# Performance work log

Measured on AMD Instinct MI355X. Metric: run time of the kernel, lower is better.

## Reference

```python
import jax, jax.numpy as jnp
import numpy as np
from jax import lax

TEMP = 65.0
CLIP_DIST = 0.01
EPS = 1e-6  # torch PairwiseDistance eps (added to the difference) and log eps
NTOKEN, NINP, NHID = 32000, 1024, 1024
SEQ_LEN, BSZ, NSAMPLES = 128, 64, 10


def setup_inputs() -> dict:
    key = jax.random.key(0)
    ks = jax.random.split(key, 7)
    data = jax.random.randint(ks[0], (SEQ_LEN, BSZ), 0, NTOKEN)
    samples = jax.random.randint(ks[1], (NSAMPLES, SEQ_LEN * BSZ), 0, NTOKEN)
    # encoder init_weights: uniform(-0.1, 0.1); RNN weights small to avoid tanh saturation
    emb_W = jax.random.uniform(ks[2], (NTOKEN, NINP), minval=-0.1, maxval=0.1, dtype=jnp.float32)
    W_ih = jax.random.normal(ks[3], (NHID, NINP), dtype=jnp.float32) * 0.03
    b_ih = jax.random.normal(ks[4], (NHID,), dtype=jnp.float32) * 0.01
    W_hh = jax.random.normal(ks[5], (NHID, NHID), dtype=jnp.float32) * 0.03
    b_hh = jax.random.normal(ks[6], (NHID,), dtype=jnp.float32) * 0.01
    return {"data": data, "samples": samples, "emb_W": emb_W,
            "W_ih": W_ih, "b_ih": b_ih, "W_hh": W_hh, "b_hh": b_hh}


def _sq_pdist(x, y):
    # torch PairwiseDistance(p=2).pow(2): ||x - y + eps||^2 (no sqrt needed)
    d = x - y + EPS
    return jnp.sum(d * d, axis=-1)


def reference(data, samples, emb_W, W_ih, b_ih, W_hh, b_hh):
    seq_len, bsz = data.shape
    nhid = W_hh.shape[0]
    emb = emb_W[data]                                  # [S, B, ninp]
    h0 = jnp.zeros((bsz, nhid), dtype=emb_W.dtype)

    def step(h, e):
        h_new = jnp.tanh(e @ W_ih.T + b_ih + h @ W_hh.T + b_hh)
        return h_new, h_new

    _, outs = lax.scan(step, h0, emb)                  # [S, B, H]
    raw = jnp.concatenate([h0[None], outs], axis=0)    # [S+1, B, H]

    # positive term: temp * ||h_t - h_{t+1}||^2, summed, averaged over seq_len
    pos = TEMP * _sq_pdist(raw[:-1], raw[1:])          # [S, B]
    loss = pos.sum() / seq_len

    prev = raw[:-1].reshape(seq_len * bsz, nhid)       # [S*B, H]
    samples_emb = emb_W[samples]                       # [ns, S*B, ninp]
    samples_W = samples_emb @ W_ih.T + b_ih            # [ns, S*B, H]
    hiddens_U = prev @ W_hh.T + b_hh                   # [S*B, H]

    out = jnp.tanh(samples_W + hiddens_U[None])        # [ns, S*B, H]
    dist = _sq_pdist(prev[None], out)                  # [ns, S*B]
    dist = jnp.clip(dist, 0.0, CLIP_DIST)
    n = seq_len * bsz
    sum_of_exp = jnp.sum(jnp.exp(-dist), axis=0) / n   # [S*B]
    loss = loss + jnp.log(sum_of_exp + EPS).sum()
    return loss
```

## Files before the change

### kernel.cpp

```cpp
#include <hip/hip_runtime.h>
#include <hip/hip_bf16.h>
#include <cmath>

typedef __bf16 bf16;
typedef __attribute__((ext_vector_type(8))) __bf16 bf16x8;
typedef __attribute__((ext_vector_type(4))) __bf16 bf16x4;
typedef __attribute__((ext_vector_type(4))) float f32x4;
typedef unsigned long long ull;

#define TEMPC 65.0f
#define EPSC 1e-6f

#define GLD_LDS16(gptr, lptr)                                                             \
    __builtin_amdgcn_global_load_lds(                                                     \
        (const __attribute__((address_space(1))) unsigned int*)(gptr),                    \
        (__attribute__((address_space(3))) unsigned int*)(lptr), 16, 0, 0)

__global__ void conv3_kernel(const float* __restrict__ e, bf16* __restrict__ eb,
                             const float* __restrict__ a, bf16* __restrict__ ab,
                             const float* __restrict__ b, bf16* __restrict__ bb)
{
    const int base   = (blockIdx.x * blockDim.x + threadIdx.x) * 4;
    const int stride = gridDim.x * blockDim.x * 4;
    for (int i = base; i < 32000 * 1024; i += stride) {
        const float4 v = *(const float4*)(e + i);
        bf16x4 o; o[0]=(bf16)v.x; o[1]=(bf16)v.y; o[2]=(bf16)v.z; o[3]=(bf16)v.w;
        *(bf16x4*)(eb + i) = o;
    }
    for (int i = base; i < 1024 * 1024; i += stride) {
        const float4 v = *(const float4*)(a + i);
        bf16x4 o; o[0]=(bf16)v.x; o[1]=(bf16)v.y; o[2]=(bf16)v.z; o[3]=(bf16)v.w;
        *(bf16x4*)(ab + i) = o;
    }
    for (int i = base; i < 1024 * 1024; i += stride) {
        const float4 v = *(const float4*)(b + i);
        bf16x4 o; o[0]=(bf16)v.x; o[1]=(bf16)v.y; o[2]=(bf16)v.z; o[3]=(bf16)v.w;
        *(bf16x4*)(bb + i) = o;
    }
}

__global__ __launch_bounds__(256, 1)
void fused_kernel(const int* __restrict__ data, const bf16* __restrict__ emb,
                  const bf16* __restrict__ Wih, const float* __restrict__ bih,
                  bf16* __restrict__ P, bf16* __restrict__ raw,
                  const bf16* __restrict__ Whh, bf16* __restrict__ XWb,
                  const float* __restrict__ bhh, bf16* __restrict__ Ust,
                  int* __restrict__ cnt, float* __restrict__ lacc)
{
    __shared__ __align__(16) char pool[147584];
    const int tid = threadIdx.x;
    const int l   = tid & 63;
    const int w   = tid >> 6;
    const int id  = blockIdx.x;

    if (id < 128) {
        bf16* Wlds = (bf16*)pool;
        char* Hlds = pool + 131072;
        const int group  = id & 7;
        const int slot   = id >> 3;
        const int jbase  = slot * 64;
        const int frow   = l & 15;
        const int kchunk = l >> 4;
        const int jglob  = jbase + w * 16 + frow;
        const int rr     = frow & 7;

        {
            const int jloc = l >> 2;
            const int csw  = ((l & 3) ^ ((l >> 3) & 3)) * 16;
            const char* gsrc = (const char*)Whh + (size_t)(jbase + w * 16 + jloc) * 2048 + csw;
            for (int kk = 0; kk < 32; ++kk)
                GLD_LDS16(gsrc + kk * 64, Wlds + (kk * 4 + w) * 512);
            asm volatile("s_waitcnt vmcnt(0)" ::: "memory");
            __syncthreads();
        }
        const float bh = bhh[jglob];

        const int ksw   = kchunk ^ ((frow >> 1) & 3);
        const bf16* wrd = Wlds + w * 512 + frow * 32 + ksw * 8;
        const char* hrd = Hlds + rr * 2064 + kchunk * 16;
        const int jpair = jglob & ~1;
        float posacc = 0.f;

        for (int t = 0; t < 128; ++t) {
            if (t > 0) {
                if (tid < 4)
                    while (__hip_atomic_load(&cnt[((t * 8 + group) * 4 + tid) * 32],
                                             __ATOMIC_RELAXED, __HIP_MEMORY_SCOPE_AGENT) < 4)
                        __builtin_amdgcn_s_sleep(1);
                __syncthreads();
            }
            const ull* hsrc8 = (const ull*)(raw + (size_t)t * 65536 + group * 8192);
            ull hv[8];
            #pragma unroll
            for (int i = 0; i < 8; ++i)
                hv[i] = __hip_atomic_load(hsrc8 + tid + i * 256,
                                          __ATOMIC_RELAXED, __HIP_MEMORY_SCOPE_AGENT);
            unsigned int xww[4];
            #pragma unroll
            for (int r = 0; r < 4; ++r) {
                const int bc = (kchunk * 4 + r) & 7;
                const size_t row = (size_t)(t * 64 + group * 8 + bc);
                xww[r] = __hip_atomic_load((const unsigned int*)(XWb + row * 1024 + jpair),
                                           __ATOMIC_RELAXED, __HIP_MEMORY_SCOPE_AGENT);
            }
            #pragma unroll
            for (int i = 0; i < 8; ++i)
                *(ull*)(Hlds + i * 2064 + tid * 8) = hv[i];
            __syncthreads();

            f32x4 acc0 = {0.f,0.f,0.f,0.f}, acc1 = {0.f,0.f,0.f,0.f};
            #pragma unroll
            for (int kk = 0; kk < 32; kk += 2) {
                bf16x8 a0 = *(const bf16x8*)(hrd + kk * 64);
                bf16x8 a1 = *(const bf16x8*)(hrd + kk * 64 + 64);
                acc0 = __builtin_amdgcn_mfma_f32_16x16x32_bf16(a0, *(const bf16x8*)(wrd + kk * 2048),       acc0, 0, 0, 0);
                acc1 = __builtin_amdgcn_mfma_f32_16x16x32_bf16(a1, *(const bf16x8*)(wrd + (kk + 1) * 2048), acc1, 0, 0, 0);
            }

            for (;;) {
                bool bad = false;
                #pragma unroll
                for (int r = 0; r < 4; ++r) bad |= (xww[r] == 0xFFFFFFFFu);
                if (!bad) break;
                #pragma unroll
                for (int r = 0; r < 4; ++r)
                    if (xww[r] == 0xFFFFFFFFu) {
                        const int bc = (kchunk * 4 + r) & 7;
                        const size_t row = (size_t)(t * 64 + group * 8 + bc);
                        xww[r] = __hip_atomic_load((const unsigned int*)(XWb + row * 1024 + jpair),
                                                   __ATOMIC_RELAXED, __HIP_MEMORY_SCOPE_AGENT);
                    }
            }

            bf16* rawN = raw + (size_t)(t + 1) * 65536;
            if (l < 32) {
                #pragma unroll
                for (int r = 0; r < 4; ++r) {
                    const int b = (l >> 4) * 4 + r;
                    const unsigned short x16 = (jglob & 1) ? (unsigned short)(xww[r] >> 16)
                                                           : (unsigned short)(xww[r] & 0xFFFF);
                    const float xwv = __builtin_bit_cast(float, (unsigned int)x16 << 16);
                    const float V = acc0[r] + acc1[r] + bh;
                    const float h = tanhf(xwv + V);
                    const size_t row = (size_t)(t * 64 + group * 8 + b);
                    Ust[row * 1024 + jglob] = (bf16)V;
                    const bf16 hb = (bf16)h;
                    const float ht = (float)*(const bf16*)(Hlds + b * 2064 + jglob * 2);
                    const float pd = ht - (float)hb + EPSC;
                    posacc += pd * pd;
                    unsigned short hs = __builtin_bit_cast(unsigned short, hb);
                    unsigned short hn = (unsigned short)__shfl_down((int)hs, 1, 64);
                    if ((frow & 1) == 0) {
                        unsigned int pack = (unsigned int)hs | ((unsigned int)hn << 16);
                        unsigned int* dst = (unsigned int*)(rawN + (size_t)(group * 8 + b) * 1024 + jglob);
                        __hip_atomic_store(dst, pack, __ATOMIC_RELAXED, __HIP_MEMORY_SCOPE_AGENT);
                    }
                }
            }
            if (t < 127) {
                __syncthreads();
                if (tid == 0)
                    __hip_atomic_fetch_add(&cnt[(((t + 1) * 8 + group) * 4 + (slot & 3)) * 32], 1,
                                           __ATOMIC_RELAXED, __HIP_MEMORY_SCOPE_AGENT);
            }
        }
        #pragma unroll
        for (int off2 = 32; off2 > 0; off2 >>= 1) posacc += __shfl_down(posacc, off2, 64);
        if (l == 0) atomicAdd(lacc, posacc * (TEMPC / 128.f));
    } else {
        bf16* As = (bf16*)pool;
        bf16* Bs = (bf16*)(pool + 16384);
        const int wr = w >> 1, wc = w & 1;
        const bool isXW = (id < 640);

        int mbase, nbase;
        const char *Asrc0, *Asrc1;
        const int r0 = w * 32 + (l >> 2);
        const int csw = ((l & 3) ^ ((l >> 3) & 3)) * 16;
        if (isXW) {
            const int q = id - 128;
            mbase = (q >> 3) * 128;
            nbase = (q & 7) * 128;
            Asrc0 = (const char*)emb + (size_t)data[mbase + r0] * 2048 + csw;
            Asrc1 = (const char*)emb + (size_t)data[mbase + r0 + 16] * 2048 + csw;
        } else {
            const int q  = id - 640;
            const int wg = (q & 7) * 250 + (q >> 3);
            mbase = (wg >> 3) * 128;
            nbase = (wg & 7) * 128;
            Asrc0 = (const char*)emb + (size_t)(mbase + r0) * 2048 + csw;
            Asrc1 = (const char*)emb + (size_t)(mbase + r0 + 16) * 2048 + csw;
        }
        const char* Bsrc0 = (const char*)Wih + (size_t)(nbase + r0) * 2048 + csw;
        const char* Bsrc1 = (const char*)Wih + (size_t)(nbase + r0 + 16) * 2048 + csw;

        const int frow  = l & 15;
        const int koffE = (((l >> 4) ^ ((frow >> 1) & 3)) * 8);
        const bf16* Ard = As + (wr * 64 + frow) * 32 + koffE;
        const bf16* Brd = Bs + (wc * 64 + frow) * 32 + koffE;

        auto stage = [&](int buf, int kb) {
            bf16* As_ = As + buf * 4096 + w * 1024;
            bf16* Bs_ = Bs + buf * 4096 + w * 1024;
            GLD_LDS16(Asrc0 + kb, As_);
            GLD_LDS16(Asrc1 + kb, As_ + 512);
            GLD_LDS16(Bsrc0 + kb, Bs_);
            GLD_LDS16(Bsrc1 + kb, Bs_ + 512);
        };

        stage(0, 0);
        stage(1, 64);

        f32x4 acc[4][4] = {};
        for (int k = 0; k < 32; ++k) {
            if (k == 31) asm volatile("s_waitcnt vmcnt(0)" ::: "memory");
            else         asm volatile("s_waitcnt vmcnt(4)" ::: "memory");
            __builtin_amdgcn_s_barrier();
            const bf16* Ab = Ard + (k & 1) * 4096;
            const bf16* Bb = Brd + (k & 1) * 4096;
            bf16x8 af[4], bfr[4];
            #pragma unroll
            for (int mt = 0; mt < 4; ++mt) af[mt]  = *(const bf16x8*)(Ab + mt * 16 * 32);
            #pragma unroll
            for (int nt = 0; nt < 4; ++nt) bfr[nt] = *(const bf16x8*)(Bb + nt * 16 * 32);
            #pragma unroll
            for (int mt = 0; mt < 4; ++mt)
                #pragma unroll
                for (int nt = 0; nt < 4; ++nt)
                    acc[mt][nt] = __builtin_amdgcn_mfma_f32_16x16x32_bf16(af[mt], bfr[nt], acc[mt][nt], 0, 0, 0);
            asm volatile("s_waitcnt lgkmcnt(0)" ::: "memory");
            __builtin_amdgcn_s_barrier();
            if (k + 2 < 32) stage(k & 1, (k + 2) * 64);
        }

        if (isXW) {
            #pragma unroll
            for (int mt = 0; mt < 4; ++mt)
                #pragma unroll
                for (int nt = 0; nt < 4; ++nt) {
                    const int colg = nbase + wc * 64 + nt * 16 + frow;
                    const float bi = bih[colg];
                    #pragma unroll
                    for (int r = 0; r < 4; ++r) {
                        const int rowg = mbase + wr * 64 + mt * 16 + (l >> 4) * 4 + r;
                        const bf16 vb = (bf16)(acc[mt][nt][r] + bi);
                        unsigned short vs = __builtin_bit_cast(unsigned short, vb);
                        unsigned short vn = (unsigned short)__shfl_down((int)vs, 1, 64);
                        if ((frow & 1) == 0) {
                            unsigned int pack = (unsigned int)vs | ((unsigned int)vn << 16);
                            __hip_atomic_store((unsigned int*)(XWb + (size_t)rowg * 1024 + colg),
                                               pack, __ATOMIC_RELAXED, __HIP_MEMORY_SCOPE_AGENT);
                        }
                    }
                }
        } else {
            #pragma unroll
            for (int mt = 0; mt < 4; ++mt)
                #pragma unroll
                for (int nt = 0; nt < 4; ++nt) {
                    const int colg = nbase + wc * 64 + nt * 16 + frow;
                    const float bi = bih[colg];
                    #pragma unroll
                    for (int r = 0; r < 4; ++r) {
                        const int rowg = mbase + wr * 64 + mt * 16 + (l >> 4) * 4 + r;
                        P[(size_t)rowg * 1024 + colg] = (bf16)(acc[mt][nt][r] + bi);
                    }
                }
        }
    }
}

__global__ __launch_bounds__(256)
void neg_kernel(const int* __restrict__ samples, const bf16* __restrict__ P,
                const bf16* __restrict__ Ust, const bf16* __restrict__ raw,
                float* __restrict__ lacc)
{
    const int l = threadIdx.x & 63;
    const int r = blockIdx.x * 4 + (threadIdx.x >> 6);
    const bf16* u  = Ust + (size_t)r * 1024;
    const bf16* pv = raw + (size_t)r * 1024;

    float uf[16], vf[16];
    {
        bf16x8 u0 = *(const bf16x8*)(u + l * 8);
        bf16x8 u1 = *(const bf16x8*)(u + 512 + l * 8);
        bf16x8 v0 = *(const bf16x8*)(pv + l * 8);
        bf16x8 v1 = *(const bf16x8*)(pv + 512 + l * 8);
        #pragma unroll
        for (int i = 0; i < 8; ++i) {
            uf[i] = (float)u0[i]; uf[8 + i] = (float)u1[i];
            vf[i] = (float)v0[i]; vf[8 + i] = (float)v1[i];
        }
    }

    float se = 0.f;
    #pragma unroll
    for (int s = 0; s < 10; ++s) {
        const int tok = samples[s * 8192 + r];
        const bf16* pr = P + (size_t)tok * 1024;
        bf16x8 p0 = *(const bf16x8*)(pr + l * 8);
        bf16x8 p1 = *(const bf16x8*)(pr + 512 + l * 8);
        float d2 = 0.f;
        #pragma unroll
        for (int i = 0; i < 8; ++i) {
            const float o0 = tanhf((float)p0[i] + uf[i]);
            const float d0 = vf[i] - o0 + EPSC;
            d2 += d0 * d0;
            const float o1 = tanhf((float)p1[i] + uf[8 + i]);
            const float d1 = vf[8 + i] - o1 + EPSC;
            d2 += d1 * d1;
        }
        #pragma unroll
        for (int off = 1; off < 64; off <<= 1)
            d2 += __shfl_xor(d2, off, 64);
        se += expf(-fminf(d2, 0.01f));
    }
    if (l == 0) atomicAdd(lacc, logf(se * (1.f / 8192.f) + EPSC));
}

__global__ void fin_kernel(const float* __restrict__ lacc, float* __restrict__ out)
{
    if (threadIdx.x == 0) out[0] = lacc[0];
}

extern "C" void kernel_launch(void* const* d_in, const int* in_sizes, int n_in,
                              void* d_out, int out_size, void* d_ws, size_t ws_size,
                              hipStream_t stream)
{
    const int*   data    = (const int*)d_in[0];
    const int*   samples = (const int*)d_in[1];
    const float* emb     = (const float*)d_in[2];
    const float* Wih     = (const float*)d_in[3];
    const float* bih     = (const float*)d_in[4];
    const float* Whh     = (const float*)d_in[5];
    const float* bhh     = (const float*)d_in[6];

    char* ws = (char*)d_ws;
    size_t off = 0;
    auto alloc = [&](size_t bytes) { void* p = ws + off; off += (bytes + 255) & ~(size_t)255; return p; };
    bf16*  emb_b = (bf16*)alloc((size_t)32000 * 1024 * 2);
    bf16*  Wih_b = (bf16*)alloc((size_t)1024 * 1024 * 2);
    bf16*  Whh_b = (bf16*)alloc((size_t)1024 * 1024 * 2);
    bf16*  P     = (bf16*)alloc((size_t)32000 * 1024 * 2);
    bf16*  XWb   = (bf16*)alloc((size_t)8192 * 1024 * 2);
    bf16*  Ust   = (bf16*)alloc((size_t)8192 * 1024 * 2);
    bf16*  raw   = (bf16*)alloc((size_t)129 * 64 * 1024 * 2);
    float* lacc  = (float*)alloc(256);
    int*   cnt   = (int*)alloc(524288);

    hipMemsetAsync(raw, 0, 64 * 1024 * 2, stream);
    hipMemsetAsync(XWb, 0xFF, (size_t)8192 * 1024 * 2, stream);
    hipMemsetAsync(lacc, 0, 256, stream);
    hipMemsetAsync(cnt,  0, 524288, stream);

    conv3_kernel<<<2048, 256, 0, stream>>>(emb, emb_b, Wih, Wih_b, Whh, Whh_b);

    fused_kernel<<<2640, 256, 0, stream>>>(data, emb_b, Wih_b, bih, P,
                                           raw, Whh_b, XWb, bhh, Ust, cnt, lacc);

    neg_kernel<<<2048, 256, 0, stream>>>(samples, P, Ust, raw, lacc);

    fin_kernel<<<1, 64, 0, stream>>>(lacc, (float*)d_out);
}
```

Before: 577.2 us.

## Fuse embedding bf16 conversion into GEMM loads and negative-sampling into persistent kernel

After: 615.3 us. 1.07x slower.

```diff
diff --git a/kernel.cpp b/kernel.cpp
--- a/kernel.cpp
+++ b/kernel.cpp
@@ -10,42 +10,44 @@
 
 #define TEMPC 65.0f
 #define EPSC 1e-6f
+#define PD_OFF 200000
 
 #define GLD_LDS16(gptr, lptr)                                                             \
     __builtin_amdgcn_global_load_lds(                                                     \
         (const __attribute__((address_space(1))) unsigned int*)(gptr),                    \
         (__attribute__((address_space(3))) unsigned int*)(lptr), 16, 0, 0)
 
-__global__ void conv3_kernel(const float* __restrict__ e, bf16* __restrict__ eb,
-                             const float* __restrict__ a, bf16* __restrict__ ab,
+__device__ __forceinline__ bf16x8 ald16(const bf16* p)
+{
+    union { ull u[2]; bf16x8 v; } c;
+    c.u[0] = __hip_atomic_load((const ull*)p,     __ATOMIC_RELAXED, __HIP_MEMORY_SCOPE_AGENT);
+    c.u[1] = __hip_atomic_load((const ull*)p + 1, __ATOMIC_RELAXED, __HIP_MEMORY_SCOPE_AGENT);
+    return c.v;
+}
+
+__global__ void conv2_kernel(const float* __restrict__ a, bf16* __restrict__ ab,
                              const float* __restrict__ b, bf16* __restrict__ bb)
 {
-    const int base   = (blockIdx.x * blockDim.x + threadIdx.x) * 4;
+    int i = (blockIdx.x * blockDim.x + threadIdx.x) * 4;
     const int stride = gridDim.x * blockDim.x * 4;
-    for (int i = base; i < 32000 * 1024; i += stride) {
-        const float4 v = *(const float4*)(e + i);
-        bf16x4 o; o[0]=(bf16)v.x; o[1]=(bf16)v.y; o[2]=(bf16)v.z; o[3]=(bf16)v.w;
-        *(bf16x4*)(eb + i) = o;
+    for (; i < 1024 * 1024; i += stride) {
+        const float4 va = *(const float4*)(a + i);
+        bf16x4 oa; oa[0]=(bf16)va.x; oa[1]=(bf16)va.y; oa[2]=(bf16)va.z; oa[3]=(bf16)va.w;
+        *(bf16x4*)(ab + i) = oa;
+        const float4 vb = *(const float4*)(b + i);
+        bf16x4 ob; ob[0]=(bf16)vb.x; ob[1]=(bf16)vb.y; ob[2]=(bf16)vb.z; ob[3]=(bf16)vb.w;
+        *(bf16x4*)(bb + i) = ob;
     }
-    for (int i = base; i < 1024 * 1024; i += stride) {
-        const float4 v = *(const float4*)(a + i);
-        bf16x4 o; o[0]=(bf16)v.x; o[1]=(bf16)v.y; o[2]=(bf16)v.z; o[3]=(bf16)v.w;
-        *(bf16x4*)(ab + i) = o;
-    }
-    for (int i = base; i < 1024 * 1024; i += stride) {
-        const float4 v = *(const float4*)(b + i);
-        bf16x4 o; o[0]=(bf16)v.x; o[1]=(bf16)v.y; o[2]=(bf16)v.z; o[3]=(bf16)v.w;
-        *(bf16x4*)(bb + i) = o;
-    }
 }
 
 __global__ __launch_bounds__(256, 1)
-void fused_kernel(const int* __restrict__ data, const bf16* __restrict__ emb,
-                  const bf16* __restrict__ Wih, const float* __restrict__ bih,
-                  bf16* __restrict__ P, bf16* __restrict__ raw,
-                  const bf16* __restrict__ Whh, bf16* __restrict__ XWb,
-                  const float* __restrict__ bhh, bf16* __restrict__ Ust,
-                  int* __restrict__ cnt, float* __restrict__ lacc)
+void fused_kernel(const int* __restrict__ data, const int* __restrict__ samples,
+                  const float* __restrict__ embf, const bf16* __restrict__ Wih,
+                  const float* __restrict__ bih, bf16* __restrict__ P,
+                  bf16* __restrict__ raw, const bf16* __restrict__ Whh,
+                  bf16* __restrict__ XWb, const float* __restrict__ bhh,
+                  bf16* __restrict__ Ust, int* __restrict__ cnt,
+                  float* __restrict__ lacc)
 {
     __shared__ __align__(16) char pool[147584];
     const int tid = threadIdx.x;
@@ -143,79 +145,97 @@
                     const float V = acc0[r] + acc1[r] + bh;
                     const float h = tanhf(xwv + V);
                     const size_t row = (size_t)(t * 64 + group * 8 + b);
-                    Ust[row * 1024 + jglob] = (bf16)V;
+                    const bf16 ub = (bf16)V;
                     const bf16 hb = (bf16)h;
                     const float ht = (float)*(const bf16*)(Hlds + b * 2064 + jglob * 2);
                     const float pd = ht - (float)hb + EPSC;
                     posacc += pd * pd;
+                    unsigned short us = __builtin_bit_cast(unsigned short, ub);
                     unsigned short hs = __builtin_bit_cast(unsigned short, hb);
+                    unsigned short un = (unsigned short)__shfl_down((int)us, 1, 64);
                     unsigned short hn = (unsigned short)__shfl_down((int)hs, 1, 64);
                     if ((frow & 1) == 0) {
-                        unsigned int pack = (unsigned int)hs | ((unsigned int)hn << 16);
-                        unsigned int* dst = (unsigned int*)(rawN + (size_t)(group * 8 + b) * 1024 + jglob);
-                        __hip_atomic_store(dst, pack, __ATOMIC_RELAXED, __HIP_MEMORY_SCOPE_AGENT);
+                        unsigned int up = (unsigned int)us | ((unsigned int)un << 16);
+                        unsigned int hp = (unsigned int)hs | ((unsigned int)hn << 16);
+                        __hip_atomic_store((unsigned int*)(Ust + row * 1024 + jglob), up,
+                                           __ATOMIC_RELAXED, __HIP_MEMORY_SCOPE_AGENT);
+                        __hip_atomic_store((unsigned int*)(rawN + (size_t)(group * 8 + b) * 1024 + jglob), hp,
+                                           __ATOMIC_RELAXED, __HIP_MEMORY_SCOPE_AGENT);
                     }
                 }
             }
-            if (t < 127) {
-                __syncthreads();
-                if (tid == 0)
-                    __hip_atomic_fetch_add(&cnt[(((t + 1) * 8 + group) * 4 + (slot & 3)) * 32], 1,
-                                           __ATOMIC_RELAXED, __HIP_MEMORY_SCOPE_AGENT);
-            }
+            __syncthreads();
+            if (tid == 0)
+                __hip_atomic_fetch_add(&cnt[(((t + 1) * 8 + group) * 4 + (slot & 3)) * 32], 1,
+                                       __ATOMIC_RELAXED, __HIP_MEMORY_SCOPE_AGENT);
         }
         #pragma unroll
         for (int off2 = 32; off2 > 0; off2 >>= 1) posacc += __shfl_down(posacc, off2, 64);
         if (l == 0) atomicAdd(lacc, posacc * (TEMPC / 128.f));
-    } else {
+    } else if (id < 2640) {
         bf16* As = (bf16*)pool;
         bf16* Bs = (bf16*)(pool + 16384);
         const int wr = w >> 1, wc = w & 1;
         const bool isXW = (id < 640);
 
         int mbase, nbase;
-        const char *Asrc0, *Asrc1;
-        const int r0 = w * 32 + (l >> 2);
-        const int csw = ((l & 3) ^ ((l >> 3) & 3)) * 16;
+        const int rla = w * 32 + (l >> 2);
+        const int g8  = ((l & 3) ^ ((l >> 3) & 3)) * 8;
+        const float *Af0, *Af1;
         if (isXW) {
             const int q = id - 128;
             mbase = (q >> 3) * 128;
             nbase = (q & 7) * 128;
-            Asrc0 = (const char*)emb + (size_t)data[mbase + r0] * 2048 + csw;
-            Asrc1 = (const char*)emb + (size_t)data[mbase + r0 + 16] * 2048 + csw;
+            Af0 = embf + (size_t)data[mbase + rla] * 1024 + g8;
+            Af1 = embf + (size_t)data[mbase + rla + 16] * 1024 + g8;
         } else {
             const int q  = id - 640;
             const int wg = (q & 7) * 250 + (q >> 3);
             mbase = (wg >> 3) * 128;
             nbase = (wg & 7) * 128;
-            Asrc0 = (const char*)emb + (size_t)(mbase + r0) * 2048 + csw;
-            Asrc1 = (const char*)emb + (size_t)(mbase + r0 + 16) * 2048 + csw;
-        }
-        const char* Bsrc0 = (const char*)Wih + (size_t)(nbase + r0) * 2048 + csw;
-        const char* Bsrc1 = (const char*)Wih + (size_t)(nbase + r0 + 16) * 2048 + csw;
-
-        const int frow  = l & 15;
-        const int koffE = (((l >> 4) ^ ((frow >> 1) & 3)) * 8);
-        const bf16* Ard = As + (wr * 64 + frow) * 32 + koffE;
-        const bf16* Brd = Bs + (wc * 64 + frow) * 32 + koffE;
-
-        auto stage = [&](int buf, int kb) {
-            bf16* As_ = As + buf * 4096 + w * 1024;
+            Af0 = embf + (size_t)(mbase + rla) * 1024 + g8;
+            Af1 = embf + (size_t)(mbase + rla + 16) * 1024 + g8;
+        }
+        const int csw = ((l & 3) ^ ((l >> 3) & 3)) * 16;
+        const char* Bsrc0 = (const char*)Wih + (size_t)(nbase + rla) * 2048 + csw;
+        const char* Bsrc1 = (const char*)Wih + (size_t)(nbase + rla + 16) * 2048 + csw;
+        char* Adst = (char*)As + w * 2048 + l * 16;
+
+        float4 fa00, fa01, fa10, fa11;
+        auto issueA = [&](int k) {
+            const float* s0 = Af0 + k * 32;
+            const float* s1 = Af1 + k * 32;
+            fa00 = *(const float4*)s0;  fa01 = *(const float4*)(s0 + 4);
+            fa10 = *(const float4*)s1;  fa11 = *(const float4*)(s1 + 4);
+        };
+        auto writeA = [&](int buf) {
+            bf16x8 o0, o1;
+            o0[0]=(bf16)fa00.x; o0[1]=(bf16)fa00.y; o0[2]=(bf16)fa00.z; o0[3]=(bf16)fa00.w;
+            o0[4]=(bf16)fa01.x; o0[5]=(bf16)fa01.y; o0[6]=(bf16)fa01.z; o0[7]=(bf16)fa01.w;
+            o1[0]=(bf16)fa10.x; o1[1]=(bf16)fa10.y; o1[2]=(bf16)fa10.z; o1[3]=(bf16)fa10.w;
+            o1[4]=(bf16)fa11.x; o1[5]=(bf16)fa11.y; o1[6]=(bf16)fa11.z; o1[7]=(bf16)fa11.w;
+            *(bf16x8*)(Adst + buf * 8192) = o0;
+            *(bf16x8*)(Adst + buf * 8192 + 1024) = o1;
+        };
+        auto stageB = [&](int buf, int kb) {
             bf16* Bs_ = Bs + buf * 4096 + w * 1024;
-            GLD_LDS16(Asrc0 + kb, As_);
-            GLD_LDS16(Asrc1 + kb, As_ + 512);
             GLD_LDS16(Bsrc0 + kb, Bs_);
             GLD_LDS16(Bsrc1 + kb, Bs_ + 512);
         };
 
-        stage(0, 0);
-        stage(1, 64);
+        const int frow  = l & 15;
+        const int koffE = ((l >> 4) ^ ((frow >> 1) & 3)) * 8;
+        const bf16* Ard = As + (wr * 64 + frow) * 32 + koffE;
+        const bf16* Brd = Bs + (wc * 64 + frow) * 32 + koffE;
+
+        issueA(0);
+        stageB(0, 0);
+        writeA(0);
+        __syncthreads();
 
         f32x4 acc[4][4] = {};
         for (int k = 0; k < 32; ++k) {
-            if (k == 31) asm volatile("s_waitcnt vmcnt(0)" ::: "memory");
-            else         asm volatile("s_waitcnt vmcnt(4)" ::: "memory");
-            __builtin_amdgcn_s_barrier();
+            if (k + 1 < 32) { issueA(k + 1); stageB((k + 1) & 1, (k + 1) * 64); }
             const bf16* Ab = Ard + (k & 1) * 4096;
             const bf16* Bb = Brd + (k & 1) * 4096;
             bf16x8 af[4], bfr[4];
@@ -228,94 +248,95 @@
                 #pragma unroll
                 for (int nt = 0; nt < 4; ++nt)
                     acc[mt][nt] = __builtin_amdgcn_mfma_f32_16x16x32_bf16(af[mt], bfr[nt], acc[mt][nt], 0, 0, 0);
-            asm volatile("s_waitcnt lgkmcnt(0)" ::: "memory");
-            __builtin_amdgcn_s_barrier();
-            if (k + 2 < 32) stage(k & 1, (k + 2) * 64);
-        }
-
-        if (isXW) {
-            #pragma unroll
-            for (int mt = 0; mt < 4; ++mt)
-                #pragma unroll
-                for (int nt = 0; nt < 4; ++nt) {
-                    const int colg = nbase + wc * 64 + nt * 16 + frow;
-                    const float bi = bih[colg];
-                    #pragma unroll
-                    for (int r = 0; r < 4; ++r) {
-                        const int rowg = mbase + wr * 64 + mt * 16 + (l >> 4) * 4 + r;
-                        const bf16 vb = (bf16)(acc[mt][nt][r] + bi);
-                        unsigned short vs = __builtin_bit_cast(unsigned short, vb);
-                        unsigned short vn = (unsigned short)__shfl_down((int)vs, 1, 64);
-                        if ((frow & 1) == 0) {
-                            unsigned int pack = (unsigned int)vs | ((unsigned int)vn << 16);
-                            __hip_atomic_store((unsigned int*)(XWb + (size_t)rowg * 1024 + colg),
-                                               pack, __ATOMIC_RELAXED, __HIP_MEMORY_SCOPE_AGENT);
-                        }
+            if (k + 1 < 32) writeA((k + 1) & 1);
+            __syncthreads();
+        }
+
+        #pragma unroll
+        for (int mt = 0; mt < 4; ++mt)
+            #pragma unroll
+            for (int nt = 0; nt < 4; ++nt) {
+                const int colg = nbase + wc * 64 + nt * 16 + frow;
+                const float bi = bih[colg];
+                #pragma unroll
+                for (int r = 0; r < 4; ++r) {
+                    const int rowg = mbase + wr * 64 + mt * 16 + (l >> 4) * 4 + r;
+                    const bf16 vb = (bf16)(acc[mt][nt][r] + bi);
+                    unsigned short vs = __builtin_bit_cast(unsigned short, vb);
+                    unsigned short vn = (unsigned short)__shfl_down((int)vs, 1, 64);
+                    if ((frow & 1) == 0) {
+                        unsigned int pack = (unsigned int)vs | ((unsigned int)vn << 16);
+                        bf16* dstbuf = isXW ? XWb : P;
+                        __hip_atomic_store((unsigned int*)(dstbuf + (size_t)rowg * 1024 + colg),
+                                           pack, __ATOMIC_RELAXED, __HIP_MEMORY_SCOPE_AGENT);
                     }
                 }
-        } else {
-            #pragma unroll
-            for (int mt = 0; mt < 4; ++mt)
-                #pragma unroll
-                for (int nt = 0; nt < 4; ++nt) {
-                    const int colg = nbase + wc * 64 + nt * 16 + frow;
-                    const float bi = bih[colg];
-                    #pragma unroll
-                    for (int r = 0; r < 4; ++r) {
-                        const int rowg = mbase + wr * 64 + mt * 16 + (l >> 4) * 4 + r;
-                        P[(size_t)rowg * 1024 + colg] = (bf16)(acc[mt][nt][r] + bi);
-                    }
+            }
+        if (!isXW) {
+            __syncthreads();
+            if (tid == 0)
+                __hip_atomic_fetch_add(&cnt[PD_OFF], 1,
+                                       __ATOMIC_RELAXED, __HIP_MEMORY_SCOPE_AGENT);
+        }
+    } else {
+        const int n  = id - 2640;
+        const int r0 = n * 16;
+        const int t  = r0 >> 6;
+        const int g0 = (r0 & 63) >> 3;
+        if (tid < 8) {
+            const int g   = g0 + (tid >> 2);
+            const int sub = tid & 3;
+            while (__hip_atomic_load(&cnt[(((t + 1) * 8 + g) * 4 + sub) * 32],
+                                     __ATOMIC_RELAXED, __HIP_MEMORY_SCOPE_AGENT) < 4)
+                __builtin_amdgcn_s_sleep(8);
+        } else if (tid == 8) {
+            while (__hip_atomic_load(&cnt[PD_OFF],
+                                     __ATOMIC_RELAXED, __HIP_MEMORY_SCOPE_AGENT) < 2000)
+                __builtin_amdgcn_s_sleep(8);
+        }
+        __syncthreads();
+
+        for (int i = 0; i < 4; ++i) {
+            const int r = r0 + w * 4 + i;
+            const bf16* u  = Ust + (size_t)r * 1024;
+            const bf16* pv = raw + (size_t)r * 1024;
+            float uf[16], vf[16];
+            {
+                bf16x8 u0 = ald16(u + l * 8);
+                bf16x8 u1 = ald16(u + 512 + l * 8);
+                bf16x8 v0 = ald16(pv + l * 8);
+                bf16x8 v1 = ald16(pv + 512 + l * 8);
+                #pragma unroll
+                for (int j = 0; j < 8; ++j) {
+                    uf[j] = (float)u0[j]; uf[8 + j] = (float)u1[j];
+                    vf[j] = (float)v0[j]; vf[8 + j] = (float)v1[j];
                 }
+            }
+            float se = 0.f;
+            #pragma unroll
+            for (int s = 0; s < 10; ++s) {
+                const int tok = samples[s * 8192 + r];
+                const bf16* pr = P + (size_t)tok * 1024;
+                bf16x8 p0 = ald16(pr + l * 8);
+                bf16x8 p1 = ald16(pr + 512 + l * 8);
+                float d2 = 0.f;
+                #pragma unroll
+                for (int j = 0; j < 8; ++j) {
+                    const float o0 = tanhf((float)p0[j] + uf[j]);
+                    const float d0 = vf[j] - o0 + EPSC;
+                    d2 += d0 * d0;
+                    const float o1 = tanhf((float)p1[j] + uf[8 + j]);
+                    const float d1 = vf[8 + j] - o1 + EPSC;
+                    d2 += d1 * d1;
+                }
+                #pragma unroll
+                for (int off = 1; off < 64; off <<= 1)
+                    d2 += __shfl_xor(d2, off, 64);
+                se += expf(-fminf(d2, 0.01f));
+            }
+            if (l == 0) atomicAdd(lacc, logf(se * (1.f / 8192.f) + EPSC));
         }
     }
-}
-
-__global__ __launch_bounds__(256)
-void neg_kernel(const int* __restrict__ samples, const bf16* __restrict__ P,
-                const bf16* __restrict__ Ust, const bf16* __restrict__ raw,
-                float* __restrict__ lacc)
-{
-    const int l = threadIdx.x & 63;
-    const int r = blockIdx.x * 4 + (threadIdx.x >> 6);
-    const bf16* u  = Ust + (size_t)r * 1024;
-    const bf16* pv = raw + (size_t)r * 1024;
-
-    float uf[16], vf[16];
-    {
-        bf16x8 u0 = *(const bf16x8*)(u + l * 8);
-        bf16x8 u1 = *(const bf16x8*)(u + 512 + l * 8);
-        bf16x8 v0 = *(const bf16x8*)(pv + l * 8);
-        bf16x8 v1 = *(const bf16x8*)(pv + 512 + l * 8);
-        #pragma unroll
-        for (int i = 0; i < 8; ++i) {
-            uf[i] = (float)u0[i]; uf[8 + i] = (float)u1[i];
-            vf[i] = (float)v0[i]; vf[8 + i] = (float)v1[i];
-        }
-    }
-
-    float se = 0.f;
-    #pragma unroll
-    for (int s = 0; s < 10; ++s) {
-        const int tok = samples[s * 8192 + r];
-        const bf16* pr = P + (size_t)tok * 1024;
-        bf16x8 p0 = *(const bf16x8*)(pr + l * 8);
-        bf16x8 p1 = *(const bf16x8*)(pr + 512 + l * 8);
-        float d2 = 0.f;
-        #pragma unroll
-        for (int i = 0; i < 8; ++i) {
-            const float o0 = tanhf((float)p0[i] + uf[i]);
-            const float d0 = vf[i] - o0 + EPSC;
-            d2 += d0 * d0;
-            const float o1 = tanhf((float)p1[i] + uf[8 + i]);
-            const float d1 = vf[8 + i] - o1 + EPSC;
-            d2 += d1 * d1;
-        }
-        #pragma unroll
-        for (int off = 1; off < 64; off <<= 1)
-            d2 += __shfl_xor(d2, off, 64);
-        se += expf(-fminf(d2, 0.01f));
-    }
-    if (l == 0) atomicAdd(lacc, logf(se * (1.f / 8192.f) + EPSC));
 }
 
 __global__ void fin_kernel(const float* __restrict__ lacc, float* __restrict__ out)
@@ -338,7 +359,6 @@
     char* ws = (char*)d_ws;
     size_t off = 0;
     auto alloc = [&](size_t bytes) { void* p = ws + off; off += (bytes + 255) & ~(size_t)255; return p; };
-    bf16*  emb_b = (bf16*)alloc((size_t)32000 * 1024 * 2);
     bf16*  Wih_b = (bf16*)alloc((size_t)1024 * 1024 * 2);
     bf16*  Whh_b = (bf16*)alloc((size_t)1024 * 1024 * 2);
     bf16*  P     = (bf16*)alloc((size_t)32000 * 1024 * 2);
@@ -346,19 +366,17 @@
     bf16*  Ust   = (bf16*)alloc((size_t)8192 * 1024 * 2);
     bf16*  raw   = (bf16*)alloc((size_t)129 * 64 * 1024 * 2);
     float* lacc  = (float*)alloc(256);
-    int*   cnt   = (int*)alloc(524288);
+    int*   cnt   = (int*)alloc(1048576);
 
     hipMemsetAsync(raw, 0, 64 * 1024 * 2, stream);
     hipMemsetAsync(XWb, 0xFF, (size_t)8192 * 1024 * 2, stream);
     hipMemsetAsync(lacc, 0, 256, stream);
-    hipMemsetAsync(cnt,  0, 524288, stream);
-
-    conv3_kernel<<<2048, 256, 0, stream>>>(emb, emb_b, Wih, Wih_b, Whh, Whh_b);
-
-    fused_kernel<<<2640, 256, 0, stream>>>(data, emb_b, Wih_b, bih, P,
+    hipMemsetAsync(cnt,  0, 1048576, stream);
+
+    conv2_kernel<<<512, 256, 0, stream>>>(Wih, Wih_b, Whh, Whh_b);
+
+    fused_kernel<<<3152, 256, 0, stream>>>(data, samples, emb, Wih_b, bih, P,
                                            raw, Whh_b, XWb, bhh, Ust, cnt, lacc);
 
-    neg_kernel<<<2048, 256, 0, stream>>>(samples, P, Ust, raw, lacc);
-
     fin_kernel<<<1, 64, 0, stream>>>(lacc, (float*)d_out);
 }
```
